# Kernel tuning notes

Hardware: AMD Instinct MI355X
Metric: run time of the kernel (lower is better)

Reference implementation:

```python
import jax, jax.numpy as jnp
import numpy as np

DX, DU = 4, 2   # dim_x, dim_u of the linear-Gaussian env
P = 8192        # num_p particles (also number of backward samples)
LOG_2PI = float(np.log(2.0 * np.pi))


def setup_inputs() -> dict:
    key = jax.random.key(0)
    ks = jax.random.split(key, 6)
    particles = jax.random.normal(ks[0], (P, DX + DU), dtype=jnp.float32)      # [x, u] per particle
    samples = jax.random.normal(ks[1], (P, DX), dtype=jnp.float32)             # next-step backward samples
    weights = 0.1 * jax.random.normal(ks[2], (P,), dtype=jnp.float32)          # incoming smoothed log-weights
    log_weights = jax.nn.log_softmax(jax.random.normal(ks[3], (P,), dtype=jnp.float32))  # forward filter log-weights
    A = 0.3 * jax.random.normal(ks[4], (DX, DX), dtype=jnp.float32)            # dynamics matrix
    B = 0.3 * jax.random.normal(ks[5], (DX, DU), dtype=jnp.float32)            # control matrix
    log_sigma = jnp.zeros((DX,), dtype=jnp.float32)                            # log std of dynamics noise
    return {"particles": particles, "samples": samples, "weights": weights,
            "log_weights": log_weights, "A": A, "B": B, "log_sigma": log_sigma}


def reference(particles, samples, weights, log_weights, A, B, log_sigma):
    # Vectorized ParticleI2cCell.backward_smoothing (Doucet et al. backward reweighing).
    dx = A.shape[0]
    x = particles[:, :dx]              # [P, dx]
    u = particles[:, dx:]              # [P, du]
    mean = x @ A.T + u @ B.T           # env dynamics mean, [P, dx]

    # Diagonal-Gaussian log-likelihood of every sample under every particle's
    # predicted next-state distribution, via the expanded squared distance so
    # we never materialize a [P, N, dx] tensor.
    inv_sigma = jnp.exp(-log_sigma)
    s = samples[:, :dx] * inv_sigma    # [N, dx] scaled
    m = mean * inv_sigma               # [P, dx] scaled
    sq = (jnp.sum(s * s, axis=-1)[None, :]
          + jnp.sum(m * m, axis=-1)[:, None]
          - 2.0 * (m @ s.T))           # [P, N] squared Mahalanobis distance
    ll = -0.5 * sq - jnp.sum(log_sigma) - 0.5 * dx * LOG_2PI  # [P, N]

    # forward_ll_norm = logsumexp(forward_ll + self.log_weights) per particle
    norm = jax.scipy.special.logsumexp(ll + log_weights[None, :], axis=1)      # [P]
    # smoothed_weights[p] = logsumexp(forward_ll + weights - norm)
    smoothed = jax.scipy.special.logsumexp(ll + weights[None, :] - norm[:, None], axis=1)  # [P]
    return smoothed
```

## Files before the change

### kernel.cpp

```cpp
#include <hip/hip_runtime.h>


constexpr int DXc = 4;
constexpr int DUc = 2;
constexpr float LOG2E = 1.4426950408889634f;
constexpr float LN2   = 0.6931471805599453f;

template <int R, int BLOCK, int JCHUNK>
__global__ __launch_bounds__(BLOCK) void pair_fused(
    const float* __restrict__ particles,
    const float* __restrict__ samples,
    const float* __restrict__ weights,
    const float* __restrict__ log_weights,
    const float* __restrict__ A,
    const float* __restrict__ B,
    const float* __restrict__ log_sigma,
    float* __restrict__ part1,
    float* __restrict__ part2,
    int P)
{
    const int tid = threadIdx.x;
    const int jc  = blockIdx.x;
    const int rowBase = blockIdx.y * (BLOCK * R);

    __shared__ __align__(16) float jds[JCHUNK * 8];

    const float K = -0.5f * LOG2E;

    float inv_s[DXc];
#pragma unroll
    for (int k = 0; k < DXc; ++k)
        inv_s[k] = __builtin_amdgcn_exp2f(-log_sigma[k] * LOG2E);

    if (tid < JCHUNK) {
        int j = jc * JCHUNK + tid;
        float4 sv = reinterpret_cast<const float4*>(samples)[j];
        float s0 = sv.x * inv_s[0], s1 = sv.y * inv_s[1];
        float s2 = sv.z * inv_s[2], s3 = sv.w * inv_s[3];
        float sn = s0*s0 + s1*s1 + s2*s2 + s3*s3;
        float4 av = make_float4(LOG2E*s0, LOG2E*s1, LOG2E*s2, LOG2E*s3);
        float4 bv = make_float4(K * sn,
                                __builtin_amdgcn_exp2f(log_weights[j] * LOG2E),
                                __builtin_amdgcn_exp2f(weights[j] * LOG2E),
                                0.f);
        reinterpret_cast<float4*>(jds)[tid * 2]     = av;
        reinterpret_cast<float4*>(jds)[tid * 2 + 1] = bv;
    }

    float m0[R], m1[R], m2[R], m3[R], acc1[R], acc2[R];
#pragma unroll
    for (int r = 0; r < R; ++r) {
        int row = rowBase + tid + r * BLOCK;
        const float2* p2 = reinterpret_cast<const float2*>(particles) + (size_t)row * 3;
        float2 x01 = p2[0], x23 = p2[1], u01 = p2[2];
        float x[4] = {x01.x, x01.y, x23.x, x23.y};
        float u[2] = {u01.x, u01.y};
        float mk[4];
#pragma unroll
        for (int k = 0; k < 4; ++k) {
            float mean =       A[k*4+0] * x[0];
            mean = fmaf(A[k*4+1], x[1], mean);
            mean = fmaf(A[k*4+2], x[2], mean);
            mean = fmaf(A[k*4+3], x[3], mean);
            mean = fmaf(B[k*2+0], u[0], mean);
            mean = fmaf(B[k*2+1], u[1], mean);
            mk[k] = mean * inv_s[k];
        }
        m0[r] = mk[0]; m1[r] = mk[1]; m2[r] = mk[2]; m3[r] = mk[3];
        acc1[r] = 0.f; acc2[r] = 0.f;
    }

    __syncthreads();

    const float4* jf = reinterpret_cast<const float4*>(jds);
#pragma unroll 4
    for (int jj = 0; jj < JCHUNK; ++jj) {
        float4 av = jf[jj * 2];
        float4 bv = jf[jj * 2 + 1];
#pragma unroll
        for (int r = 0; r < R; ++r) {
            float t = fmaf(m0[r], av.x, bv.x);
            t = fmaf(m1[r], av.y, t);
            t = fmaf(m2[r], av.z, t);
            t = fmaf(m3[r], av.w, t);
            float e = __builtin_amdgcn_exp2f(t);
            acc1[r] = fmaf(e, bv.y, acc1[r]);
            acc2[r] = fmaf(e, bv.z, acc2[r]);
        }
    }

#pragma unroll
    for (int r = 0; r < R; ++r) {
        int row = rowBase + tid + r * BLOCK;
        part1[(size_t)jc * P + row] = acc1[r];
        part2[(size_t)jc * P + row] = acc2[r];
    }
}

__global__ __launch_bounds__(256) void reduce_kernel(
    const float* __restrict__ part1,
    const float* __restrict__ part2,
    float* __restrict__ out, int P, int NJ)
{
    const int rl = threadIdx.x & 63;
    const int sl = threadIdx.x >> 6;
    const int row = blockIdx.x * 64 + rl;

    float s1 = 0.f, s2 = 0.f;
    for (int nj = sl; nj < NJ; nj += 4) {
        s1 += part1[(size_t)nj * P + row];
        s2 += part2[(size_t)nj * P + row];
    }
    __shared__ float l1[4][64], l2[4][64];
    l1[sl][rl] = s1; l2[sl][rl] = s2;
    __syncthreads();
    if (sl == 0) {
        float t1 = ((l1[0][rl] + l1[1][rl]) + l1[2][rl]) + l1[3][rl];
        float t2 = ((l2[0][rl] + l2[1][rl]) + l2[2][rl]) + l2[3][rl];
        out[row] = (__builtin_amdgcn_logf(t2) - __builtin_amdgcn_logf(t1)) * LN2;
    }
}

extern "C" void kernel_launch(void* const* d_in, const int* in_sizes, int n_in,
                              void* d_out, int out_size, void* d_ws, size_t ws_size,
                              hipStream_t stream)
{
    const float* particles   = (const float*)d_in[0];
    const float* samples     = (const float*)d_in[1];
    const float* weights     = (const float*)d_in[2];
    const float* log_weights = (const float*)d_in[3];
    const float* A           = (const float*)d_in[4];
    const float* B           = (const float*)d_in[5];
    const float* log_sigma   = (const float*)d_in[6];

    const int P = in_sizes[2];

    int NJ = 128;
    while (NJ > 32 && (size_t)2 * NJ * P * sizeof(float) > ws_size)
        NJ >>= 1;

    float* part1 = (float*)d_ws;
    float* part2 = part1 + (size_t)NJ * P;

    constexpr int R = 4, BLOCK = 256;
    dim3 grid(NJ, P / (R * BLOCK));

    switch (NJ) {
    case 128:
        pair_fused<R, BLOCK, 64><<<grid, BLOCK, 0, stream>>>(
            particles, samples, weights, log_weights, A, B, log_sigma,
            part1, part2, P);
        break;
    case 64:
        pair_fused<R, BLOCK, 128><<<grid, BLOCK, 0, stream>>>(
            particles, samples, weights, log_weights, A, B, log_sigma,
            part1, part2, P);
        break;
    default:
        pair_fused<R, BLOCK, 256><<<grid, BLOCK, 0, stream>>>(
            particles, samples, weights, log_weights, A, B, log_sigma,
            part1, part2, P);
        break;
    }

    reduce_kernel<<<P / 64, 256, 0, stream>>>(part1, part2, (float*)d_out, P, NJ);
}
```

Before: 32.33 us.

## Split precompute kernel and use packed FMA with 8 rows per thread

Moves the per-sample and per-particle preprocessing into a separate kernel that writes a packed sample table and struct-of-arrays scaled means. The pair kernel then only loads these, processes two rows per packed v2f FMA with eight rows per thread, and prefetches the next shared-memory entry. Grid shape and chunk size change too, and each chunk defaults to 32 samples. The goal is to halve the FMA instruction count and remove redundant per-block setup. The cost is an extra kernel launch, more partial-sum workspace and traffic, and higher register pressure.

```diff
diff --git a/kernel.cpp b/kernel.cpp
--- a/kernel.cpp
+++ b/kernel.cpp
@@ -1,13 +1,17 @@
 #include <hip/hip_runtime.h>
 
 
-constexpr int DXc = 4;
-constexpr int DUc = 2;
+typedef float v2f __attribute__((ext_vector_type(2)));
+
 constexpr float LOG2E = 1.4426950408889634f;
 constexpr float LN2   = 0.6931471805599453f;
 
-template <int R, int BLOCK, int JCHUNK>
-__global__ __launch_bounds__(BLOCK) void pair_fused(
+__device__ __forceinline__ v2f splat2(float x) { v2f r; r[0] = x; r[1] = x; return r; }
+__device__ __forceinline__ v2f pkfma(v2f a, v2f b, v2f c) {
+    return __builtin_elementwise_fma(a, b, c);
+}
+
+__global__ __launch_bounds__(256) void precompute_kernel(
     const float* __restrict__ particles,
     const float* __restrict__ samples,
     const float* __restrict__ weights,
@@ -15,85 +19,110 @@
     const float* __restrict__ A,
     const float* __restrict__ B,
     const float* __restrict__ log_sigma,
+    float* __restrict__ jdata,
+    float* __restrict__ msoa,
+    int P)
+{
+    int i = blockIdx.x * blockDim.x + threadIdx.x;
+    if (i >= P) return;
+
+    const float K = -0.5f * LOG2E;
+
+    float inv_s[4];
+#pragma unroll
+    for (int k = 0; k < 4; ++k)
+        inv_s[k] = __builtin_amdgcn_exp2f(-log_sigma[k] * LOG2E);
+
+    float4 sv = reinterpret_cast<const float4*>(samples)[i];
+    float s0 = sv.x * inv_s[0], s1 = sv.y * inv_s[1];
+    float s2 = sv.z * inv_s[2], s3 = sv.w * inv_s[3];
+    float sn = s0*s0 + s1*s1 + s2*s2 + s3*s3;
+
+    float4* jd = reinterpret_cast<float4*>(jdata + (size_t)i * 8);
+    jd[0] = make_float4(LOG2E*s0, LOG2E*s1, LOG2E*s2, LOG2E*s3);
+    jd[1] = make_float4(K * sn,
+                        __builtin_amdgcn_exp2f(log_weights[i] * LOG2E),
+                        __builtin_amdgcn_exp2f(weights[i] * LOG2E),
+                        0.f);
+
+    const float2* p2 = reinterpret_cast<const float2*>(particles) + (size_t)i * 3;
+    float2 x01 = p2[0], x23 = p2[1], u01 = p2[2];
+    float x[4] = {x01.x, x01.y, x23.x, x23.y};
+    float u[2] = {u01.x, u01.y};
+#pragma unroll
+    for (int k = 0; k < 4; ++k) {
+        float mean =       A[k*4+0] * x[0];
+        mean = fmaf(A[k*4+1], x[1], mean);
+        mean = fmaf(A[k*4+2], x[2], mean);
+        mean = fmaf(A[k*4+3], x[3], mean);
+        mean = fmaf(B[k*2+0], u[0], mean);
+        mean = fmaf(B[k*2+1], u[1], mean);
+        msoa[(size_t)k * P + i] = mean * inv_s[k];
+    }
+}
+
+template <int R2, int BLOCK, int JCHUNK>
+__global__ __launch_bounds__(BLOCK) void pair_kernel(
+    const float* __restrict__ jdata,
+    const float* __restrict__ msoa,
     float* __restrict__ part1,
     float* __restrict__ part2,
     int P)
 {
     const int tid = threadIdx.x;
     const int jc  = blockIdx.x;
-    const int rowBase = blockIdx.y * (BLOCK * R);
-
-    __shared__ __align__(16) float jds[JCHUNK * 8];
-
-    const float K = -0.5f * LOG2E;
-
-    float inv_s[DXc];
-#pragma unroll
-    for (int k = 0; k < DXc; ++k)
-        inv_s[k] = __builtin_amdgcn_exp2f(-log_sigma[k] * LOG2E);
-
+    const int rowBase = blockIdx.y * (BLOCK * 2 * R2);
+
+    __shared__ __align__(16) float4 jds[JCHUNK * 2];
     if (tid < JCHUNK) {
-        int j = jc * JCHUNK + tid;
-        float4 sv = reinterpret_cast<const float4*>(samples)[j];
-        float s0 = sv.x * inv_s[0], s1 = sv.y * inv_s[1];
-        float s2 = sv.z * inv_s[2], s3 = sv.w * inv_s[3];
-        float sn = s0*s0 + s1*s1 + s2*s2 + s3*s3;
-        float4 av = make_float4(LOG2E*s0, LOG2E*s1, LOG2E*s2, LOG2E*s3);
-        float4 bv = make_float4(K * sn,
-                                __builtin_amdgcn_exp2f(log_weights[j] * LOG2E),
-                                __builtin_amdgcn_exp2f(weights[j] * LOG2E),
-                                0.f);
-        reinterpret_cast<float4*>(jds)[tid * 2]     = av;
-        reinterpret_cast<float4*>(jds)[tid * 2 + 1] = bv;
-    }
-
-    float m0[R], m1[R], m2[R], m3[R], acc1[R], acc2[R];
-#pragma unroll
-    for (int r = 0; r < R; ++r) {
-        int row = rowBase + tid + r * BLOCK;
-        const float2* p2 = reinterpret_cast<const float2*>(particles) + (size_t)row * 3;
-        float2 x01 = p2[0], x23 = p2[1], u01 = p2[2];
-        float x[4] = {x01.x, x01.y, x23.x, x23.y};
-        float u[2] = {u01.x, u01.y};
-        float mk[4];
-#pragma unroll
-        for (int k = 0; k < 4; ++k) {
-            float mean =       A[k*4+0] * x[0];
-            mean = fmaf(A[k*4+1], x[1], mean);
-            mean = fmaf(A[k*4+2], x[2], mean);
-            mean = fmaf(A[k*4+3], x[3], mean);
-            mean = fmaf(B[k*2+0], u[0], mean);
-            mean = fmaf(B[k*2+1], u[1], mean);
-            mk[k] = mean * inv_s[k];
-        }
-        m0[r] = mk[0]; m1[r] = mk[1]; m2[r] = mk[2]; m3[r] = mk[3];
-        acc1[r] = 0.f; acc2[r] = 0.f;
+        const float4* src = reinterpret_cast<const float4*>(jdata) +
+                            (size_t)(jc * JCHUNK + tid) * 2;
+        jds[tid * 2]     = src[0];
+        jds[tid * 2 + 1] = src[1];
+    }
+
+    v2f m0[R2], m1[R2], m2[R2], m3[R2], a1[R2], a2[R2];
+#pragma unroll
+    for (int p = 0; p < R2; ++p) {
+        int r0 = rowBase + 2 * tid + p * (2 * BLOCK);
+        m0[p] = *reinterpret_cast<const v2f*>(msoa + 0 * (size_t)P + r0);
+        m1[p] = *reinterpret_cast<const v2f*>(msoa + 1 * (size_t)P + r0);
+        m2[p] = *reinterpret_cast<const v2f*>(msoa + 2 * (size_t)P + r0);
+        m3[p] = *reinterpret_cast<const v2f*>(msoa + 3 * (size_t)P + r0);
+        a1[p] = splat2(0.f);
+        a2[p] = splat2(0.f);
     }
 
     __syncthreads();
 
-    const float4* jf = reinterpret_cast<const float4*>(jds);
+    float4 av = jds[0], bv = jds[1];
 #pragma unroll 4
     for (int jj = 0; jj < JCHUNK; ++jj) {
-        float4 av = jf[jj * 2];
-        float4 bv = jf[jj * 2 + 1];
-#pragma unroll
-        for (int r = 0; r < R; ++r) {
-            float t = fmaf(m0[r], av.x, bv.x);
-            t = fmaf(m1[r], av.y, t);
-            t = fmaf(m2[r], av.z, t);
-            t = fmaf(m3[r], av.w, t);
-            float e = __builtin_amdgcn_exp2f(t);
-            acc1[r] = fmaf(e, bv.y, acc1[r]);
-            acc2[r] = fmaf(e, bv.z, acc2[r]);
+        float4 avn, bvn;
+        if (jj + 1 < JCHUNK) { avn = jds[2*jj + 2]; bvn = jds[2*jj + 3]; }
+        v2f va0 = splat2(av.x), va1 = splat2(av.y);
+        v2f va2 = splat2(av.z), va3 = splat2(av.w);
+        v2f vc  = splat2(bv.x), velw = splat2(bv.y), vew = splat2(bv.z);
+#pragma unroll
+        for (int p = 0; p < R2; ++p) {
+            v2f t = pkfma(m0[p], va0, vc);
+            t = pkfma(m1[p], va1, t);
+            t = pkfma(m2[p], va2, t);
+            t = pkfma(m3[p], va3, t);
+            v2f e;
+            e[0] = __builtin_amdgcn_exp2f(t[0]);
+            e[1] = __builtin_amdgcn_exp2f(t[1]);
+            a1[p] = pkfma(e, velw, a1[p]);
+            a2[p] = pkfma(e, vew,  a2[p]);
         }
-    }
-
-#pragma unroll
-    for (int r = 0; r < R; ++r) {
-        int row = rowBase + tid + r * BLOCK;
-        part1[(size_t)jc * P + row] = acc1[r];
-        part2[(size_t)jc * P + row] = acc2[r];
+        av = avn; bv = bvn;
+    }
+
+#pragma unroll
+    for (int p = 0; p < R2; ++p) {
+        int r0 = rowBase + 2 * tid + p * (2 * BLOCK);
+        *reinterpret_cast<v2f*>(part1 + (size_t)jc * P + r0) = a1[p];
+        *reinterpret_cast<v2f*>(part2 + (size_t)jc * P + r0) = a2[p];
     }
 }
 
@@ -135,31 +164,39 @@
 
     const int P = in_sizes[2];
 
-    int NJ = 128;
-    while (NJ > 32 && (size_t)2 * NJ * P * sizeof(float) > ws_size)
-        NJ >>= 1;
-
-    float* part1 = (float*)d_ws;
+    float* jdata = (float*)d_ws;
+    float* msoa  = jdata + (size_t)P * 8;
+    float* partbase = msoa + (size_t)P * 4;
+
+    size_t base_bytes = (size_t)P * 12 * sizeof(float);
+    int JCHUNK = 32;
+    int NJ = P / JCHUNK;
+    while (JCHUNK < 128 &&
+           base_bytes + (size_t)2 * NJ * P * sizeof(float) > ws_size) {
+        JCHUNK <<= 1;
+        NJ = P / JCHUNK;
+    }
+    float* part1 = partbase;
     float* part2 = part1 + (size_t)NJ * P;
 
-    constexpr int R = 4, BLOCK = 256;
-    dim3 grid(NJ, P / (R * BLOCK));
-
-    switch (NJ) {
-    case 128:
-        pair_fused<R, BLOCK, 64><<<grid, BLOCK, 0, stream>>>(
-            particles, samples, weights, log_weights, A, B, log_sigma,
-            part1, part2, P);
+    precompute_kernel<<<(P + 255) / 256, 256, 0, stream>>>(
+        particles, samples, weights, log_weights, A, B, log_sigma,
+        jdata, msoa, P);
+
+    constexpr int R2 = 4, BLOCK = 256;
+    dim3 grid(NJ, P / (2 * R2 * BLOCK));
+    switch (JCHUNK) {
+    case 32:
+        pair_kernel<R2, BLOCK, 32><<<grid, BLOCK, 0, stream>>>(
+            jdata, msoa, part1, part2, P);
         break;
     case 64:
-        pair_fused<R, BLOCK, 128><<<grid, BLOCK, 0, stream>>>(
-            particles, samples, weights, log_weights, A, B, log_sigma,
-            part1, part2, P);
+        pair_kernel<R2, BLOCK, 64><<<grid, BLOCK, 0, stream>>>(
+            jdata, msoa, part1, part2, P);
         break;
     default:
-        pair_fused<R, BLOCK, 256><<<grid, BLOCK, 0, stream>>>(
-            particles, samples, weights, log_weights, A, B, log_sigma,
-            part1, part2, P);
+        pair_kernel<R2, BLOCK, 128><<<grid, BLOCK, 0, stream>>>(
+            jdata, msoa, part1, part2, P);
         break;
     }
 
```

Result: slower. 46.23 us (+43.0%).
